# Kernel optimization log

Hardware: AMD Instinct MI355X
Metric: run time of the kernel (lower is better)

Reference implementation:

```python
import jax, jax.numpy as jnp
import numpy as np

SWITCH_W = 30.0
TOL = 5
DECAY = 0.7
FP_PEN = 10.0
INV_PEN = 100.0
CLASS_W = jnp.array([1.0, 1.0, SWITCH_W, SWITCH_W], dtype=jnp.float32)


def setup_inputs() -> dict:
    key = jax.random.key(0)
    k1, k2, k3 = jax.random.split(key, 3)
    B, S, C = 512, 8192, 4
    logits = jax.random.normal(k1, (B, S, C), dtype=jnp.float32)
    labels = jax.random.randint(k2, (B, S), 0, 4, dtype=jnp.int32)
    # sprinkle ignore_index (-100) positions like real padded sequences
    drop = jax.random.uniform(k3, (B, S)) < 0.05
    labels = jnp.where(drop, jnp.int32(-100), labels)
    return {"logits": logits, "labels": labels}


def _mode_multiplier(labels, preds):
    """Sequential state machine over time; carry = (pred_mode, true_mode) per batch row."""
    B, S = labels.shape

    def step(carry, xs):
        pm, tm = carry
        lab, pred = xs  # [B] each
        valid = lab != -100
        # invalid transition penalty on predicted switches
        bad = ((pred == 2) & (pm == 0)) | ((pred == 3) & (pm == 1))
        pen = jnp.where(valid & bad, INV_PEN, 1.0)
        new_pm = jnp.where(valid, jnp.where((pred == 0) | (pred == 2), 0, 1), pm)
        # reward correct mode switches (true label agrees with pred switch)
        good = ((lab == 2) & (tm == 1) & (pred == 2)) | ((lab == 3) & (tm == 0) & (pred == 3))
        bonus = jnp.where(valid & good, 0.1, 1.0)
        new_tm = jnp.where(valid & ((lab == 0) | (lab == 2)), 0,
                           jnp.where(valid & ((lab == 1) | (lab == 3)), 1, tm))
        return (new_pm, new_tm), pen * bonus

    init = (jnp.zeros((B,), jnp.int32), jnp.zeros((B,), jnp.int32))
    _, mult = jax.lax.scan(step, init, (labels.T, preds.T))
    return mult.T  # [B, S]


def _nearest_dist(mask):
    """For each position, distance to nearest True in the same row; BIG if none."""
    B, S = mask.shape
    BIG = jnp.int32(S + TOL + 2)

    def f(c, m):
        c = jnp.where(m, jnp.int32(0), jnp.minimum(c + 1, BIG))
        return c, c

    init = jnp.full((B,), BIG, jnp.int32)
    _, fwd = jax.lax.scan(f, init, mask.T)
    _, bwd = jax.lax.scan(f, init, mask[:, ::-1].T)
    return jnp.minimum(fwd.T, bwd.T[:, ::-1])


def _loss(logits, labels):
    preds = jnp.argmax(logits, axis=-1).astype(jnp.int32)
    valid = labels != -100
    labs = jnp.where(valid, labels, 0)
    logp = jax.nn.log_softmax(logits, axis=-1)
    ce = -jnp.take_along_axis(logp, labs[..., None], axis=-1)[..., 0] * CLASS_W[labs]

    mult = _mode_multiplier(labels, preds)
    for c in (2, 3):
        true_m = labels == c
        pred_m = preds == c
        d_true = _nearest_dist(true_m)
        d_pred = _nearest_dist(pred_m)
        has_true = true_m.any(axis=1, keepdims=True)
        has_pred = pred_m.any(axis=1, keepdims=True)
        # multipliers at predicted-switch positions
        mp = jnp.where(
            pred_m,
            jnp.where(
                has_true,
                jnp.where(d_true == 0, 0.1,
                          jnp.where(d_true <= TOL, DECAY ** d_true.astype(jnp.float32), FP_PEN)),
                FP_PEN * 2.0),
            1.0)
        # multipliers at true-switch positions
        mt = jnp.where(
            true_m,
            jnp.where(has_pred, jnp.where(d_pred > TOL, 2.0, 1.0), 3.0),
            1.0)
        mult = mult * mp * mt

    vf = valid.astype(ce.dtype)
    total = (ce * mult * vf).sum()
    return total / jnp.maximum(vf.sum(), 1.0)


def reference(logits, labels):
    return _loss(logits, labels)
```

## Files before the change

kernel.cpp:

```cpp
#include <hip/hip_runtime.h>
#include <math.h>

#define BROWS 512
#define SLEN  8192
#define NT    512
#define CHUNK (SLEN / NT)
#define NWRD  (SLEN / 32)
#define MWRD  (NWRD + 2)

__device__ __forceinline__ int win_dist(const unsigned int* __restrict__ M, int t) {
    int sI = t + 27;
    int w  = sI >> 5;
    int off = sI & 31;
    unsigned long long val =
        ((unsigned long long)M[w] | ((unsigned long long)M[w + 1] << 32)) >> off;
    unsigned int win = (unsigned int)val & 0x7FFu;
    if (win & 32u) return 0;
    unsigned int dn = win & 31u;
    unsigned int up = (win >> 6) & 31u;
    int d = 99;
    if (dn) d = 5 - (31 - __clz((int)dn));
    if (up) { int du = __ffs((int)up); if (du < d) d = du; }
    return d;
}

__device__ __forceinline__ float decay_pow(int d) {
    return (d == 1) ? 0.7f : (d == 2) ? 0.49f : (d == 3) ? 0.343f
         : (d == 4) ? 0.2401f : 0.16807f;
}

__global__ __launch_bounds__(NT) void row_loss_kernel(
    const float* __restrict__ logits, const int* __restrict__ labels,
    double* __restrict__ ws_sum, unsigned int* __restrict__ ws_cnt)
{
    __shared__ float         s_ce[SLEN];
    __shared__ unsigned char s_pk[SLEN];
    __shared__ unsigned int  s_m[4][MWRD];
    __shared__ unsigned int  s_scan[NT];
    __shared__ unsigned int  s_flags;
    __shared__ double        s_red[NT / 64];
    __shared__ unsigned int  s_redc[NT / 64];

    const int row = blockIdx.x;
    const int tid = threadIdx.x;

    for (int i = tid; i < 4 * MWRD; i += NT) ((unsigned int*)s_m)[i] = 0u;
    if (tid == 0) s_flags = 0u;
    __syncthreads();

    const float4* lg4 = (const float4*)(logits + (size_t)row * SLEN * 4);
    const int*    lb  = labels + (size_t)row * SLEN;

    for (int k = 0; k < CHUNK; ++k) {
        int t = k * NT + tid;
        float4 v = lg4[t];
        int lab = lb[t];
        int pred = 0; float best = v.x;
        if (v.y > best) { best = v.y; pred = 1; }
        if (v.z > best) { best = v.z; pred = 2; }
        if (v.w > best) { best = v.w; pred = 3; }
        bool valid = (lab != -100);
        int l = valid ? (lab & 3) : 0;
        float se = __expf(v.x - best) + __expf(v.y - best) +
                   __expf(v.z - best) + __expf(v.w - best);
        float lse = best + __logf(se);
        float xl = (l == 0) ? v.x : (l == 1) ? v.y : (l == 2) ? v.z : v.w;
        float wc = (l >= 2) ? 30.0f : 1.0f;
        s_ce[t] = valid ? (lse - xl) * wc : 0.0f;
        s_pk[t] = (unsigned char)(pred | (l << 2) | (valid ? 16 : 0));
    }
    __syncthreads();

    const int base = tid * CHUNK;
    unsigned int mt2 = 0, mp2 = 0, mt3 = 0, mp3 = 0;
    unsigned int summary = 0;
    for (int i = 0; i < CHUNK; ++i) {
        unsigned int pk = s_pk[base + i];
        int pred = pk & 3, l = (pk >> 2) & 3;
        bool valid = (pk & 16) != 0;
        if (pred == 2) mp2 |= 1u << i;
        if (pred == 3) mp3 |= 1u << i;
        if (valid && l == 2) mt2 |= 1u << i;
        if (valid && l == 3) mt3 |= 1u << i;
        if (valid) summary = 4u | (unsigned)(pred & 1) | ((unsigned)(l & 1) << 1);
    }
    {
        int wi = 1 + (tid >> 1);
        int sh = (tid & 1) * 16;
        if (mt2) atomicOr(&s_m[0][wi], mt2 << sh);
        if (mp2) atomicOr(&s_m[1][wi], mp2 << sh);
        if (mt3) atomicOr(&s_m[2][wi], mt3 << sh);
        if (mp3) atomicOr(&s_m[3][wi], mp3 << sh);
        unsigned int fl = (mt2 ? 1u : 0u) | (mp2 ? 2u : 0u) |
                          (mt3 ? 4u : 0u) | (mp3 ? 8u : 0u);
        if (fl) atomicOr(&s_flags, fl);
    }
    s_scan[tid] = summary;
    __syncthreads();

    for (int step = 1; step < NT; step <<= 1) {
        unsigned int v = s_scan[tid];
        unsigned int o = (tid >= step) ? s_scan[tid - step] : 0u;
        unsigned int nv = (v & 4u) ? v : o;
        __syncthreads();
        s_scan[tid] = nv;
        __syncthreads();
    }

    unsigned int pre = (tid > 0) ? s_scan[tid - 1] : 0u;
    int pm = (int)(pre & 1u), tm = (int)((pre >> 1) & 1u);
    unsigned int flags = s_flags;
    const bool hasT2 = flags & 1u, hasP2 = flags & 2u;
    const bool hasT3 = flags & 4u, hasP3 = flags & 8u;

    float acc = 0.0f;
    int cnt = 0;
    for (int i = 0; i < CHUNK; ++i) {
        int t = base + i;
        unsigned int pk = s_pk[t];
        int pred = pk & 3, l = (pk >> 2) & 3;
        bool valid = (pk & 16) != 0;
        float m = 1.0f;
        if (valid) {
            bool bad = (pred == 2 && pm == 0) || (pred == 3 && pm == 1);
            if (bad) m *= 100.0f;
            bool good = (l == 2 && tm == 1 && pred == 2) ||
                        (l == 3 && tm == 0 && pred == 3);
            if (good) m *= 0.1f;
            pm = pred & 1;
            tm = l & 1;
            cnt++;
        }
        if (pred == 2) {
            if (!hasT2) m *= 20.0f;
            else { int d = win_dist(s_m[0], t);
                   m *= (d == 0) ? 0.1f : (d <= 5) ? decay_pow(d) : 10.0f; }
        }
        if (valid && l == 2) {
            if (!hasP2) m *= 3.0f;
            else if (win_dist(s_m[1], t) > 5) m *= 2.0f;
        }
        if (pred == 3) {
            if (!hasT3) m *= 20.0f;
            else { int d = win_dist(s_m[2], t);
                   m *= (d == 0) ? 0.1f : (d <= 5) ? decay_pow(d) : 10.0f; }
        }
        if (valid && l == 3) {
            if (!hasP3) m *= 3.0f;
            else if (win_dist(s_m[3], t) > 5) m *= 2.0f;
        }
        acc += s_ce[t] * m;
    }

    double dacc = (double)acc;
    for (int o = 32; o > 0; o >>= 1) {
        dacc += __shfl_down(dacc, o);
        cnt  += __shfl_down(cnt, o);
    }
    int wid = tid >> 6, lane = tid & 63;
    if (lane == 0) { s_red[wid] = dacc; s_redc[wid] = (unsigned int)cnt; }
    __syncthreads();
    if (tid == 0) {
        double tot = 0.0; unsigned int c = 0;
        for (int i = 0; i < NT / 64; ++i) { tot += s_red[i]; c += s_redc[i]; }
        atomicAdd(ws_sum, tot);
        atomicAdd(ws_cnt, c);
    }
}

__global__ void finalize_kernel(const double* __restrict__ ws_sum,
                                const unsigned int* __restrict__ ws_cnt,
                                float* __restrict__ out)
{
    double c = (double)(*ws_cnt);
    if (c < 1.0) c = 1.0;
    out[0] = (float)(*ws_sum / c);
}

extern "C" void kernel_launch(void* const* d_in, const int* in_sizes, int n_in,
                              void* d_out, int out_size, void* d_ws, size_t ws_size,
                              hipStream_t stream) {
    const float* logits = (const float*)d_in[0];
    const int*   labels = (const int*)d_in[1];
    float* out = (float*)d_out;
    double* wsd = (double*)d_ws;
    unsigned int* wsc = (unsigned int*)(wsd + 1);

    hipMemsetAsync(d_ws, 0, 16, stream);
    row_loss_kernel<<<BROWS, NT, 0, stream>>>(logits, labels, wsd, wsc);
    finalize_kernel<<<1, 1, 0, stream>>>(wsd, wsc, out);
}
```

Measured before the change: 133.4 us.

## Use 1024-thread blocks, shuffle-based carry scan, padded CE buffer, per-row partials

New measurement: 115.9 us. -13.2%, faster.

```diff
diff --git a/kernel.cpp b/kernel.cpp
--- a/kernel.cpp
+++ b/kernel.cpp
@@ -3,10 +3,11 @@
 
 #define BROWS 512
 #define SLEN  8192
-#define NT    512
+#define NT    1024
 #define CHUNK (SLEN / NT)
 #define NWRD  (SLEN / 32)
 #define MWRD  (NWRD + 2)
+#define CEPAD (SLEN + SLEN/8)
 
 __device__ __forceinline__ int win_dist(const unsigned int* __restrict__ M, int t) {
     int sI = t + 27;
@@ -29,28 +30,31 @@
          : (d == 4) ? 0.2401f : 0.16807f;
 }
 
-__global__ __launch_bounds__(NT) void row_loss_kernel(
+__global__ __launch_bounds__(NT, 8) void row_loss_kernel(
     const float* __restrict__ logits, const int* __restrict__ labels,
-    double* __restrict__ ws_sum, unsigned int* __restrict__ ws_cnt)
+    double* __restrict__ psum, unsigned int* __restrict__ pcnt)
 {
-    __shared__ float         s_ce[SLEN];
+    __shared__ float         s_ce[CEPAD];
     __shared__ unsigned char s_pk[SLEN];
     __shared__ unsigned int  s_m[4][MWRD];
-    __shared__ unsigned int  s_scan[NT];
+    __shared__ unsigned int  s_wave[16];
+    __shared__ unsigned int  s_wavex[16];
     __shared__ unsigned int  s_flags;
-    __shared__ double        s_red[NT / 64];
-    __shared__ unsigned int  s_redc[NT / 64];
-
-    const int row = blockIdx.x;
-    const int tid = threadIdx.x;
+    __shared__ double        s_red[16];
+    __shared__ int           s_redc[16];
+
+    const int row  = blockIdx.x;
+    const int tid  = threadIdx.x;
+    const int lane = tid & 63;
+    const int wid  = tid >> 6;
 
     for (int i = tid; i < 4 * MWRD; i += NT) ((unsigned int*)s_m)[i] = 0u;
     if (tid == 0) s_flags = 0u;
-    __syncthreads();
 
     const float4* lg4 = (const float4*)(logits + (size_t)row * SLEN * 4);
     const int*    lb  = labels + (size_t)row * SLEN;
 
+    #pragma unroll
     for (int k = 0; k < CHUNK; ++k) {
         int t = k * NT + tid;
         float4 v = lg4[t];
@@ -66,7 +70,7 @@
         float lse = best + __logf(se);
         float xl = (l == 0) ? v.x : (l == 1) ? v.y : (l == 2) ? v.z : v.w;
         float wc = (l >= 2) ? 30.0f : 1.0f;
-        s_ce[t] = valid ? (lse - xl) * wc : 0.0f;
+        s_ce[t + (t >> 3)] = valid ? (lse - xl) * wc : 0.0f;
         s_pk[t] = (unsigned char)(pred | (l << 2) | (valid ? 16 : 0));
     }
     __syncthreads();
@@ -74,6 +78,7 @@
     const int base = tid * CHUNK;
     unsigned int mt2 = 0, mp2 = 0, mt3 = 0, mp3 = 0;
     unsigned int summary = 0;
+    #pragma unroll
     for (int i = 0; i < CHUNK; ++i) {
         unsigned int pk = s_pk[base + i];
         int pred = pk & 3, l = (pk >> 2) & 3;
@@ -85,29 +90,45 @@
         if (valid) summary = 4u | (unsigned)(pred & 1) | ((unsigned)(l & 1) << 1);
     }
     {
-        int wi = 1 + (tid >> 1);
-        int sh = (tid & 1) * 16;
+        int wi = 1 + (tid >> 2);
+        int sh = (tid & 3) * 8;
         if (mt2) atomicOr(&s_m[0][wi], mt2 << sh);
         if (mp2) atomicOr(&s_m[1][wi], mp2 << sh);
         if (mt3) atomicOr(&s_m[2][wi], mt3 << sh);
         if (mp3) atomicOr(&s_m[3][wi], mp3 << sh);
+    }
+    {
         unsigned int fl = (mt2 ? 1u : 0u) | (mp2 ? 2u : 0u) |
                           (mt3 ? 4u : 0u) | (mp3 ? 8u : 0u);
-        if (fl) atomicOr(&s_flags, fl);
-    }
-    s_scan[tid] = summary;
-    __syncthreads();
-
-    for (int step = 1; step < NT; step <<= 1) {
-        unsigned int v = s_scan[tid];
-        unsigned int o = (tid >= step) ? s_scan[tid - step] : 0u;
-        unsigned int nv = (v & 4u) ? v : o;
-        __syncthreads();
-        s_scan[tid] = nv;
-        __syncthreads();
-    }
-
-    unsigned int pre = (tid > 0) ? s_scan[tid - 1] : 0u;
+        #pragma unroll
+        for (int s = 32; s > 0; s >>= 1) fl |= __shfl_xor(fl, s);
+        if (lane == 0 && fl) atomicOr(&s_flags, fl);
+    }
+
+    unsigned int inc = summary;
+    #pragma unroll
+    for (int st = 1; st < 64; st <<= 1) {
+        unsigned int o = __shfl_up(inc, st);
+        if (lane >= st && !(inc & 4u)) inc = o;
+    }
+    unsigned int exc = __shfl_up(inc, 1);
+    if (lane == 0) exc = 0u;
+    if (lane == 63) s_wave[wid] = inc;
+    __syncthreads();
+    if (wid == 0) {
+        unsigned int wv = (lane < 16) ? s_wave[lane] : 0u;
+        #pragma unroll
+        for (int st = 1; st < 16; st <<= 1) {
+            unsigned int o = __shfl_up(wv, st);
+            if (lane >= st && !(wv & 4u)) wv = o;
+        }
+        unsigned int wex = __shfl_up(wv, 1);
+        if (lane == 0) wex = 0u;
+        if (lane < 16) s_wavex[lane] = wex;
+    }
+    __syncthreads();
+
+    unsigned int pre = (exc & 4u) ? exc : s_wavex[wid];
     int pm = (int)(pre & 1u), tm = (int)((pre >> 1) & 1u);
     unsigned int flags = s_flags;
     const bool hasT2 = flags & 1u, hasP2 = flags & 2u;
@@ -115,6 +136,7 @@
 
     float acc = 0.0f;
     int cnt = 0;
+    #pragma unroll
     for (int i = 0; i < CHUNK; ++i) {
         int t = base + i;
         unsigned int pk = s_pk[t];
@@ -149,32 +171,49 @@
             if (!hasP3) m *= 3.0f;
             else if (win_dist(s_m[3], t) > 5) m *= 2.0f;
         }
-        acc += s_ce[t] * m;
+        acc += s_ce[tid * 9 + i] * m;
     }
 
     double dacc = (double)acc;
+    #pragma unroll
     for (int o = 32; o > 0; o >>= 1) {
         dacc += __shfl_down(dacc, o);
         cnt  += __shfl_down(cnt, o);
     }
-    int wid = tid >> 6, lane = tid & 63;
-    if (lane == 0) { s_red[wid] = dacc; s_redc[wid] = (unsigned int)cnt; }
+    if (lane == 0) { s_red[wid] = dacc; s_redc[wid] = cnt; }
     __syncthreads();
     if (tid == 0) {
         double tot = 0.0; unsigned int c = 0;
-        for (int i = 0; i < NT / 64; ++i) { tot += s_red[i]; c += s_redc[i]; }
-        atomicAdd(ws_sum, tot);
-        atomicAdd(ws_cnt, c);
-    }
-}
-
-__global__ void finalize_kernel(const double* __restrict__ ws_sum,
-                                const unsigned int* __restrict__ ws_cnt,
-                                float* __restrict__ out)
+        #pragma unroll
+        for (int i = 0; i < 16; ++i) { tot += s_red[i]; c += (unsigned int)s_redc[i]; }
+        psum[row] = tot;
+        pcnt[row] = c;
+    }
+}
+
+__global__ __launch_bounds__(512) void finalize_kernel(
+    const double* __restrict__ psum, const unsigned int* __restrict__ pcnt,
+    float* __restrict__ out)
 {
-    double c = (double)(*ws_cnt);
-    if (c < 1.0) c = 1.0;
-    out[0] = (float)(*ws_sum / c);
+    __shared__ double       sd[8];
+    __shared__ unsigned int sc[8];
+    int tid = threadIdx.x, lane = tid & 63, wid = tid >> 6;
+    double v = psum[tid];
+    unsigned int c = pcnt[tid];
+    #pragma unroll
+    for (int o = 32; o > 0; o >>= 1) {
+        v += __shfl_down(v, o);
+        c += __shfl_down(c, o);
+    }
+    if (lane == 0) { sd[wid] = v; sc[wid] = c; }
+    __syncthreads();
+    if (tid == 0) {
+        double t = 0.0; unsigned int cc = 0;
+        #pragma unroll
+        for (int i = 0; i < 8; ++i) { t += sd[i]; cc += sc[i]; }
+        double d = (cc > 0u) ? (double)cc : 1.0;
+        out[0] = (float)(t / d);
+    }
 }
 
 extern "C" void kernel_launch(void* const* d_in, const int* in_sizes, int n_in,
@@ -183,10 +222,9 @@
     const float* logits = (const float*)d_in[0];
     const int*   labels = (const int*)d_in[1];
     float* out = (float*)d_out;
-    double* wsd = (double*)d_ws;
-    unsigned int* wsc = (unsigned int*)(wsd + 1);
-
-    hipMemsetAsync(d_ws, 0, 16, stream);
-    row_loss_kernel<<<BROWS, NT, 0, stream>>>(logits, labels, wsd, wsc);
-    finalize_kernel<<<1, 1, 0, stream>>>(wsd, wsc, out);
-}
+    double* psum = (double*)d_ws;
+    unsigned int* pcnt = (unsigned int*)(psum + BROWS);
+
+    row_loss_kernel<<<BROWS, NT, 0, stream>>>(logits, labels, psum, pcnt);
+    finalize_kernel<<<1, 512, 0, stream>>>(psum, pcnt, out);
+}
```
